# Kernel tuning notes

Hardware: AMD Instinct MI355X
Metric: run time of the kernel (lower is better)

The kernel has to match this reference:

```python
import jax, jax.numpy as jnp
import numpy as np

N_NODES = 100000
N_EDGES = 1600000
VOCAB = 15000
D_IN = 128
D_HID = 128
N_GRAPHS = 16


def setup_inputs() -> dict:
    key = jax.random.key(0)
    ks = jax.random.split(key, 16)
    stdv = 1.0 / np.sqrt(D_HID)
    inp = {
        "word_ids": jax.random.randint(ks[0], (N_NODES,), 0, VOCAB),
        "edge_src": jax.random.randint(ks[1], (N_EDGES,), 0, N_NODES),
        "edge_dst": jax.random.randint(ks[2], (N_EDGES,), 0, N_NODES),
        "edge_weight": jax.random.uniform(ks[3], (N_EDGES,), dtype=jnp.float32),
        "norm": jax.random.uniform(ks[4], (N_NODES,), dtype=jnp.float32),
        "graph_id": jnp.sort(jax.random.randint(ks[5], (N_NODES,), 0, N_GRAPHS)),
        "y_data": jax.random.uniform(ks[6], (N_GRAPHS,), dtype=jnp.float32),
        # learned params
        "word_embeds": jax.random.normal(ks[7], (VOCAB, D_IN), dtype=jnp.float32) * 0.05,
        "W0": jax.random.uniform(ks[8], (D_IN, D_HID), minval=-stdv, maxval=stdv, dtype=jnp.float32),
        "b0": jax.random.uniform(ks[9], (D_HID,), minval=-stdv, maxval=stdv, dtype=jnp.float32),
        "W1": jax.random.uniform(ks[10], (D_HID, D_HID), minval=-stdv, maxval=stdv, dtype=jnp.float32),
        "b1": jax.random.uniform(ks[11], (D_HID,), minval=-stdv, maxval=stdv, dtype=jnp.float32),
        "Wout": jax.random.uniform(ks[12], (D_HID, 1), minval=-stdv, maxval=stdv, dtype=jnp.float32),
        "bout": jax.random.uniform(ks[13], (1,), minval=-stdv, maxval=stdv, dtype=jnp.float32),
    }
    return inp


def _gcn_layer(h, W, b, norm, edge_src, edge_dst, edge_weight):
    # h: [N, d_in] -> [N, d_out]
    h = h @ W                                   # dense projection
    h = h * norm[:, None]                       # pre-aggregation norm
    msg = h[edge_src] * edge_weight[:, None]    # u_mul_e   [E, d]
    h = jax.ops.segment_sum(msg, edge_dst, num_segments=N_NODES)  # sum agg
    h = h * norm[:, None]                       # post-aggregation norm
    return jax.nn.relu(h + b)


def reference(word_ids, edge_src, edge_dst, edge_weight, norm, graph_id, y_data,
              word_embeds, W0, b0, W1, b1, Wout, bout):
    h = word_embeds[word_ids]                   # [N, D_IN]
    h = _gcn_layer(h, W0, b0, norm, edge_src, edge_dst, edge_weight)
    h = _gcn_layer(h, W1, b1, norm, edge_src, edge_dst, edge_weight)
    # per-graph max pooling (dgl.max_nodes)
    g = jax.ops.segment_max(h, graph_id, num_segments=N_GRAPHS)   # [B, D_HID]
    z = g @ Wout + bout                          # [B, 1] logits
    zf = z.reshape(-1)
    # binary_cross_entropy_with_logits, mean reduction (numerically stable)
    loss = jnp.mean(jnp.maximum(zf, 0.0) - zf * y_data + jnp.log1p(jnp.exp(-jnp.abs(zf))))
    y_pred = jax.nn.sigmoid(z)
    return loss, y_pred
```

## Files before the change

### kernel.cpp

```cpp
#include <hip/hip_runtime.h>
#include <math.h>

#define D 128
#define NG 16
#define NBINS 512
#define CHUNK 2048
#define CAPB 4608

typedef unsigned int uint;
typedef unsigned short ushort;
typedef unsigned long long u64;
typedef __attribute__((ext_vector_type(8))) short bf16x8;
typedef __attribute__((ext_vector_type(4))) float f32x4;

__device__ __forceinline__ ushort f32_to_bf16(float f) {
    uint b = __float_as_uint(f);
    b += 0x7fffu + ((b >> 16) & 1u);
    return (ushort)(b >> 16);
}
__device__ __forceinline__ uint pack_bf16x2(float lo, float hi) {
    return (uint)f32_to_bf16(lo) | ((uint)f32_to_bf16(hi) << 16);
}

__global__ __launch_bounds__(256) void k_binA(
    const int* __restrict__ esrc, const int* __restrict__ edst,
    const float* __restrict__ ew, const float* __restrict__ norm,
    u64* __restrict__ binned, int* __restrict__ loc_off,
    int* __restrict__ bin_cnt, int ne, int width)
{
    __shared__ int hist[NBINS], lscan[NBINS], lcur[NBINS];
    __shared__ int ws4[4];
    __shared__ u64 stage[CHUNK];
    const int tid = threadIdx.x;
    const int base = blockIdx.x * CHUNK;
    const int count = min(CHUNK, ne - base);

    hist[tid] = 0; hist[tid + 256] = 0;
    __syncthreads();

    int s[8], bn[8], dl[8]; float c[8];
    #pragma unroll
    for (int i = 0; i < 8; ++i) {
        int li = i * 256 + tid;
        bn[i] = -1;
        if (li < count) {
            int e = base + li;
            s[i] = esrc[e];
            int d = edst[e];
            bn[i] = d / width;
            dl[i] = d - bn[i] * width;
            c[i] = ew[e] * norm[s[i]];
            atomicAdd(&hist[bn[i]], 1);
        }
    }
    __syncthreads();

    {
        int lane = tid & 63, w = tid >> 6;
        int h0 = hist[2 * tid], h1 = hist[2 * tid + 1];
        int sum = h0 + h1, x = sum;
        for (int dlt = 1; dlt < 64; dlt <<= 1) {
            int t2 = __shfl_up(x, dlt);
            if (lane >= dlt) x += t2;
        }
        if (lane == 63) ws4[w] = x;
        __syncthreads();
        if (tid == 0) { int run = 0; for (int i = 0; i < 4; ++i) { int t3 = ws4[i]; ws4[i] = run; run += t3; } }
        __syncthreads();
        int b0 = ws4[w] + (x - sum);
        lscan[2 * tid] = b0;       lscan[2 * tid + 1] = b0 + h0;
        lcur[2 * tid] = b0;        lcur[2 * tid + 1] = b0 + h0;
    }
    __syncthreads();

    int* lo = loc_off + (size_t)blockIdx.x * (NBINS + 1);
    lo[tid] = lscan[tid]; lo[tid + 256] = lscan[tid + 256];
    if (tid == 0) lo[NBINS] = count;
    if (hist[tid])       atomicAdd(&bin_cnt[tid], hist[tid]);
    if (hist[tid + 256]) atomicAdd(&bin_cnt[tid + 256], hist[tid + 256]);

    #pragma unroll
    for (int i = 0; i < 8; ++i) {
        if (bn[i] >= 0) {
            int pos = atomicAdd(&lcur[bn[i]], 1);
            uint packed = (uint)s[i] | ((uint)dl[i] << 24);
            stage[pos] = ((u64)__float_as_uint(c[i]) << 32) | packed;
        }
    }
    __syncthreads();

    u64* outp = binned + (size_t)blockIdx.x * CHUNK;
    for (int j = tid; j < count; j += 256) outp[j] = stage[j];
}

__global__ __launch_bounds__(1024) void k_scan_top(int* __restrict__ bsum, int nb)
{
    int tid = threadIdx.x, lane = tid & 63, w = tid >> 6;
    int v = tid < nb ? bsum[tid] : 0;
    int x = v;
    for (int d = 1; d < 64; d <<= 1) {
        int t = __shfl_up(x, d);
        if (lane >= d) x += t;
    }
    __shared__ int ws[16];
    if (lane == 63) ws[w] = x;
    __syncthreads();
    if (tid == 0) { int run = 0; for (int i = 0; i < 16; ++i) { int t = ws[i]; ws[i] = run; run += t; } }
    __syncthreads();
    x += ws[w];
    if (tid < nb) bsum[tid] = x - v;
}

__global__ __launch_bounds__(256) void k_binB(
    const u64* __restrict__ binned, const int* __restrict__ loc_off,
    const int* __restrict__ bin_off, int* __restrict__ off,
    int2* __restrict__ csr, int n, int ne, int width, int nA)
{
    __shared__ u64 stA[CAPB];
    __shared__ int hist[256], cur[256];
    __shared__ int wsum[4];
    __shared__ int sTotal;
    const int tid = threadIdx.x;
    const int bin = blockIdx.x;
    const int d0 = bin * width;
    const int dcount = min(n - d0, width);
    const int base = bin_off[bin];

    if (tid == 0) sTotal = 0;
    hist[tid] = 0;
    __syncthreads();

    if (dcount > 0) {
        for (int f = tid; f < nA; f += 256) {
            const int* lo = loc_off + (size_t)f * (NBINS + 1);
            int a = lo[bin], b = lo[bin + 1];
            int len = b - a;
            if (len > 0) {
                int st = atomicAdd(&sTotal, len);
                const u64* src = binned + (size_t)f * CHUNK + a;
                for (int k = 0; k < len; ++k) {
                    u64 r = src[k];
                    stA[st + k] = r;
                    atomicAdd(&hist[(int)((r >> 24) & 0xFF)], 1);
                }
            }
        }
    }
    __syncthreads();
    const int cnt = sTotal;

    {
        int lane = tid & 63, w = tid >> 6;
        int v = hist[tid], x = v;
        for (int dlt = 1; dlt < 64; dlt <<= 1) {
            int t2 = __shfl_up(x, dlt);
            if (lane >= dlt) x += t2;
        }
        if (lane == 63) wsum[w] = x;
        __syncthreads();
        if (tid == 0) { int run = 0; for (int i = 0; i < 4; ++i) { int t3 = wsum[i]; wsum[i] = run; run += t3; } }
        __syncthreads();
        int ex = wsum[w] + x - v;
        cur[tid] = ex;
        if (tid < dcount) off[d0 + tid] = base + ex;
    }
    if (tid == 0 && dcount > 0 && d0 + dcount == n) off[n] = base + cnt;
    __syncthreads();

    for (int i = tid; i < cnt; i += 256) {
        u64 r = stA[i];
        int dl = (int)((r >> 24) & 0xFF);
        int pos = atomicAdd(&cur[dl], 1);
        csr[base + pos] = make_int2((int)(r & 0xFFFFFF), (int)(r >> 32));
    }
}

__global__ __launch_bounds__(256) void k_cvt_bf16(
    const float* __restrict__ src, ushort* __restrict__ dst, int nelem)
{
    int i = (blockIdx.x * 256 + threadIdx.x) * 4;
    if (i + 3 < nelem) {
        float4 v = *reinterpret_cast<const float4*>(src + i);
        ushort4 o;
        o.x = f32_to_bf16(v.x); o.y = f32_to_bf16(v.y);
        o.z = f32_to_bf16(v.z); o.w = f32_to_bf16(v.w);
        *reinterpret_cast<ushort4*>(dst + i) = o;
    } else {
        for (int k = 0; k < 4 && i + k < nelem; ++k) dst[i + k] = f32_to_bf16(src[i + k]);
    }
}

__global__ __launch_bounds__(256) void k_wfrag(
    const float* __restrict__ W, ushort* __restrict__ Wf)
{
    int t = blockIdx.x * 256 + threadIdx.x;
    if (t >= 2048) return;
    int lane = t & 63, tile = t >> 6;
    int ks = tile & 3, nt = tile >> 2;
    int col = nt * 16 + (lane & 15);
    int k0 = ks * 32 + (lane >> 4) * 8;
    ushort* dst = Wf + (size_t)t * 8;
    #pragma unroll
    for (int j = 0; j < 8; ++j)
        dst[j] = f32_to_bf16(W[(k0 + j) * D + col]);
}

__global__ __launch_bounds__(256) void k_agg_bf16(
    const int* __restrict__ off, const int2* __restrict__ csr,
    const int* __restrict__ wid, const ushort* __restrict__ tab,
    ushort* __restrict__ outbf, int n)
{
    int row = blockIdx.x * 8 + (threadIdx.x >> 5);
    if (row >= n) return;
    int q = threadIdx.x & 31;
    int h = q >> 4;
    int c8 = (q & 15) * 8;
    int j0 = off[row], j1 = off[row + 1];
    float acc[8] = {0.f, 0.f, 0.f, 0.f, 0.f, 0.f, 0.f, 0.f};

    for (int jb = j0; jb < j1; jb += 32) {
        int m = min(32, j1 - jb);
        int2 p = make_int2(0, 0);
        if (q < m) {
            p = csr[jb + q];
            if (wid) p.x = wid[p.x];
        }
        int t = 0;
        for (; t + 8 <= m; t += 8) {
            uint4 u[4]; float wv[4];
            #pragma unroll
            for (int k = 0; k < 4; ++k) {
                int eh = t + 2 * k + h;
                int sv = __shfl(p.x, eh, 32);
                wv[k] = __int_as_float(__shfl(p.y, eh, 32));
                u[k] = *reinterpret_cast<const uint4*>(tab + (size_t)sv * D + c8);
            }
            #pragma unroll
            for (int k = 0; k < 4; ++k) {
                acc[0] = fmaf(__uint_as_float(u[k].x << 16),          wv[k], acc[0]);
                acc[1] = fmaf(__uint_as_float(u[k].x & 0xffff0000u),  wv[k], acc[1]);
                acc[2] = fmaf(__uint_as_float(u[k].y << 16),          wv[k], acc[2]);
                acc[3] = fmaf(__uint_as_float(u[k].y & 0xffff0000u),  wv[k], acc[3]);
                acc[4] = fmaf(__uint_as_float(u[k].z << 16),          wv[k], acc[4]);
                acc[5] = fmaf(__uint_as_float(u[k].z & 0xffff0000u),  wv[k], acc[5]);
                acc[6] = fmaf(__uint_as_float(u[k].w << 16),          wv[k], acc[6]);
                acc[7] = fmaf(__uint_as_float(u[k].w & 0xffff0000u),  wv[k], acc[7]);
            }
        }
        for (; t < m; t += 2) {
            int eh = t + h;
            int sv = __shfl(p.x, eh, 32);
            float wvv = __int_as_float(__shfl(p.y, eh, 32));
            uint4 u = *reinterpret_cast<const uint4*>(tab + (size_t)sv * D + c8);
            acc[0] = fmaf(__uint_as_float(u.x << 16),         wvv, acc[0]);
            acc[1] = fmaf(__uint_as_float(u.x & 0xffff0000u), wvv, acc[1]);
            acc[2] = fmaf(__uint_as_float(u.y << 16),         wvv, acc[2]);
            acc[3] = fmaf(__uint_as_float(u.y & 0xffff0000u), wvv, acc[3]);
            acc[4] = fmaf(__uint_as_float(u.z << 16),         wvv, acc[4]);
            acc[5] = fmaf(__uint_as_float(u.z & 0xffff0000u), wvv, acc[5]);
            acc[6] = fmaf(__uint_as_float(u.w << 16),         wvv, acc[6]);
            acc[7] = fmaf(__uint_as_float(u.w & 0xffff0000u), wvv, acc[7]);
        }
    }
    #pragma unroll
    for (int i = 0; i < 8; ++i) acc[i] += __shfl_xor(acc[i], 16, 32);
    if (h == 0) {
        uint4 o;
        o.x = pack_bf16x2(acc[0], acc[1]);
        o.y = pack_bf16x2(acc[2], acc[3]);
        o.z = pack_bf16x2(acc[4], acc[5]);
        o.w = pack_bf16x2(acc[6], acc[7]);
        *reinterpret_cast<uint4*>(outbf + (size_t)row * D + c8) = o;
    }
}

__device__ __forceinline__ void gemm_core_16x128(
    const ushort* __restrict__ aggbf, const ushort* __restrict__ Wf,
    int rowbase, int lane, int n, f32x4 acc[8])
{
    int arow = rowbase + (lane & 15);
    const bf16x8* WfV = reinterpret_cast<const bf16x8*>(Wf);
    #pragma unroll
    for (int ks = 0; ks < 4; ++ks) {
        bf16x8 af = {0, 0, 0, 0, 0, 0, 0, 0};
        if (arow < n) {
            int k0 = ks * 32 + (lane >> 4) * 8;
            af = *reinterpret_cast<const bf16x8*>(aggbf + (size_t)arow * D + k0);
        }
        #pragma unroll
        for (int nt = 0; nt < 8; ++nt) {
            bf16x8 bf = WfV[(nt * 4 + ks) * 64 + lane];
            acc[nt] = __builtin_amdgcn_mfma_f32_16x16x32_bf16(af, bf, acc[nt], 0, 0, 0);
        }
    }
}

__global__ __launch_bounds__(256) void k_gemm_mfma_post(
    const ushort* __restrict__ aggbf, const ushort* __restrict__ Wf,
    const float* __restrict__ norm, const float* __restrict__ b,
    ushort* __restrict__ outbf, int n)
{
    int lane = threadIdx.x & 63;
    int w = threadIdx.x >> 6;
    int rowbase = blockIdx.x * 64 + w * 16;
    f32x4 acc[8] = {};
    gemm_core_16x128(aggbf, Wf, rowbase, lane, n, acc);

    int r0 = rowbase + (lane >> 4) * 4;
    float nrm[4];
    #pragma unroll
    for (int i = 0; i < 4; ++i) nrm[i] = (r0 + i < n) ? norm[r0 + i] : 0.f;
    #pragma unroll
    for (int nt = 0; nt < 8; ++nt) {
        int col = nt * 16 + (lane & 15);
        float bc = b[col];
        #pragma unroll
        for (int i = 0; i < 4; ++i) {
            int r = r0 + i;
            if (r < n) {
                float v = fmaxf(fmaf(acc[nt][i], nrm[i], bc), 0.f);
                outbf[(size_t)r * D + col] = f32_to_bf16(v);
            }
        }
    }
}

__global__ __launch_bounds__(256) void k_gemm_mfma_segmax(
    const ushort* __restrict__ aggbf, const ushort* __restrict__ Wf,
    const float* __restrict__ norm, const float* __restrict__ b,
    const int* __restrict__ gid, unsigned* __restrict__ g, int n)
{
    __shared__ float sh[64][132];
    __shared__ int sgid[64];
    int lane = threadIdx.x & 63;
    int w = threadIdx.x >> 6;
    int rowbase = blockIdx.x * 64 + w * 16;
    f32x4 acc[8] = {};
    gemm_core_16x128(aggbf, Wf, rowbase, lane, n, acc);

    int r0 = rowbase + (lane >> 4) * 4;
    int lr0 = w * 16 + (lane >> 4) * 4;
    float nrm[4];
    #pragma unroll
    for (int i = 0; i < 4; ++i) nrm[i] = (r0 + i < n) ? norm[r0 + i] : 0.f;
    #pragma unroll
    for (int nt = 0; nt < 8; ++nt) {
        int col = nt * 16 + (lane & 15);
        float bc = b[col];
        #pragma unroll
        for (int i = 0; i < 4; ++i) {
            float v = (r0 + i < n) ? fmaxf(fmaf(acc[nt][i], nrm[i], bc), 0.f) : 0.f;
            sh[lr0 + i][col] = v;
        }
    }
    if (threadIdx.x < 64) {
        int r = blockIdx.x * 64 + threadIdx.x;
        sgid[threadIdx.x] = (r < n) ? gid[r] : -1;
    }
    __syncthreads();

    if (threadIdx.x < D) {
        int c = threadIdx.x;
        int glo = 0x7fffffff, ghi = -1;
        #pragma unroll
        for (int i = 0; i < 64; ++i) {
            int gv = sgid[i];
            if (gv >= 0) { glo = min(glo, gv); ghi = max(ghi, gv); }
        }
        for (int gr = glo; gr <= ghi; ++gr) {
            float m = 0.f;
            #pragma unroll
            for (int i = 0; i < 64; ++i)
                if (sgid[i] == gr) m = fmaxf(m, sh[i][c]);
            if (m > 0.f) atomicMax(&g[gr * D + c], __float_as_uint(m));
        }
    }
}

__global__ __launch_bounds__(1024) void k_final(
    const unsigned* __restrict__ g, const float* __restrict__ Wout,
    const float* __restrict__ bout, const float* __restrict__ y,
    float* __restrict__ out)
{
    __shared__ float zs[NG];
    int wave = threadIdx.x >> 6, lane = threadIdx.x & 63;
    float acc = 0.f;
    for (int c = lane; c < D; c += 64)
        acc += __uint_as_float(g[wave * D + c]) * Wout[c];
    for (int off2 = 32; off2; off2 >>= 1) acc += __shfl_down(acc, off2);
    if (lane == 0) {
        float z = acc + bout[0];
        zs[wave] = z;
        out[1 + wave] = 1.f / (1.f + expf(-z));
    }
    __syncthreads();
    if (threadIdx.x == 0) {
        float loss = 0.f;
        for (int i = 0; i < NG; ++i) {
            float z = zs[i];
            loss += fmaxf(z, 0.f) - z * y[i] + log1pf(expf(-fabsf(z)));
        }
        out[0] = loss / NG;
    }
}

extern "C" void kernel_launch(void* const* d_in, const int* in_sizes, int n_in,
                              void* d_out, int out_size, void* d_ws, size_t ws_size,
                              hipStream_t stream) {
    const int*   word_ids = (const int*)  d_in[0];
    const int*   esrc     = (const int*)  d_in[1];
    const int*   edst     = (const int*)  d_in[2];
    const float* ew       = (const float*)d_in[3];
    const float* norm     = (const float*)d_in[4];
    const int*   gid      = (const int*)  d_in[5];
    const float* y        = (const float*)d_in[6];
    const float* embeds   = (const float*)d_in[7];
    const float* W0       = (const float*)d_in[8];
    const float* b0       = (const float*)d_in[9];
    const float* W1       = (const float*)d_in[10];
    const float* b1       = (const float*)d_in[11];
    const float* Wout     = (const float*)d_in[12];
    const float* bout     = (const float*)d_in[13];

    const int n  = in_sizes[0];
    const int ne = in_sizes[1];
    const int vocab = in_sizes[7] / D;
    float* out = (float*)d_out;

    const int nA = (ne + CHUNK - 1) / CHUNK;
    const int width = (n + NBINS - 1) / NBINS;

    ushort* aggbf = (ushort*)d_ws;
    int*    off   = (int*)(aggbf + (size_t)n * D);
    int*    bcnt  = off + (n + 1);
    int*    loff  = bcnt + NBINS;
    uintptr_t bin_addr = ((uintptr_t)(loff + (size_t)nA * (NBINS + 1)) + 15) & ~(uintptr_t)15;
    u64*    binned = (u64*)bin_addr;
    int2*   csr   = (int2*)(binned + (size_t)nA * CHUNK);
    ushort* h1    = (ushort*)(csr + ne);
    ushort* emb16 = h1 + (size_t)n * D;
    unsigned* g   = (unsigned*)(emb16 + (size_t)vocab * D);
    uintptr_t wf_addr = ((uintptr_t)(g + NG * D) + 15) & ~(uintptr_t)15;
    ushort* w0f = (ushort*)wf_addr;
    ushort* w1f = w0f + D * D;

    const dim3 blk(256);
    const int ablocks = (n + 7) / 8;
    const int mblocks = (n + 63) / 64;

    hipMemsetAsync(bcnt, 0, NBINS * sizeof(int), stream);
    k_binA<<<nA, blk, 0, stream>>>(esrc, edst, ew, norm, binned, loff, bcnt, ne, width);
    k_scan_top<<<1, 1024, 0, stream>>>(bcnt, NBINS);
    k_binB<<<NBINS, blk, 0, stream>>>(binned, loff, bcnt, off, csr, n, ne, width, nA);

    k_cvt_bf16<<<(vocab * D / 4 + 255) / 256, blk, 0, stream>>>(embeds, emb16, vocab * D);
    k_wfrag<<<8, blk, 0, stream>>>(W0, w0f);
    k_wfrag<<<8, blk, 0, stream>>>(W1, w1f);

    k_agg_bf16<<<ablocks, blk, 0, stream>>>(off, csr, word_ids, emb16, aggbf, n);
    k_gemm_mfma_post<<<mblocks, blk, 0, stream>>>(aggbf, w0f, norm, b0, h1, n);

    k_agg_bf16<<<ablocks, blk, 0, stream>>>(off, csr, nullptr, h1, aggbf, n);
    hipMemsetAsync(g, 0, NG * D * sizeof(unsigned), stream);
    k_gemm_mfma_segmax<<<mblocks, blk, 0, stream>>>(aggbf, w1f, norm, b1, gid, g, n);

    k_final<<<1, 1024, 0, stream>>>(g, Wout, bout, y, out);
}
```

Baseline: 259.8 us.

## Quantize layer-1 activations to int8 with per-row scales for second aggregation

The first GEMM epilogue now computes a per-row max, writes int8-quantized activations plus a float scale per row instead of bf16. A new aggregation kernel gathers the int8 rows, dequantizes with the source row's scale folded into the edge weight, and accumulates in fp32. This halves the bytes gathered per edge in the second message-passing pass, which is dominated by random row reads. The cost is reduced precision (int8, ReLU outputs only) and an extra scale load per edge.

```diff
diff --git a/kernel.cpp b/kernel.cpp
--- a/kernel.cpp
+++ b/kernel.cpp
@@ -20,6 +20,9 @@
 }
 __device__ __forceinline__ uint pack_bf16x2(float lo, float hi) {
     return (uint)f32_to_bf16(lo) | ((uint)f32_to_bf16(hi) << 16);
+}
+__device__ __forceinline__ float sb(uint u) {
+    return (float)(int)(signed char)(u & 0xffu);
 }
 
 __global__ __launch_bounds__(256) void k_binA(
@@ -274,6 +277,74 @@
     }
 }
 
+__global__ __launch_bounds__(256) void k_agg_q8(
+    const int* __restrict__ off, const int2* __restrict__ csr,
+    const char* __restrict__ tab8, const float* __restrict__ scale,
+    ushort* __restrict__ outbf, int n)
+{
+    int row = blockIdx.x * 8 + (threadIdx.x >> 5);
+    if (row >= n) return;
+    int q = threadIdx.x & 31;
+    int h = q >> 4;
+    int c8 = (q & 15) * 8;
+    int j0 = off[row], j1 = off[row + 1];
+    float acc[8] = {0.f, 0.f, 0.f, 0.f, 0.f, 0.f, 0.f, 0.f};
+
+    for (int jb = j0; jb < j1; jb += 32) {
+        int m = min(32, j1 - jb);
+        int2 p = make_int2(0, 0);
+        if (q < m) p = csr[jb + q];
+        int t = 0;
+        for (; t + 8 <= m; t += 8) {
+            uint2 u[4]; float wv[4];
+            #pragma unroll
+            for (int k = 0; k < 4; ++k) {
+                int eh = t + 2 * k + h;
+                int sv = __shfl(p.x, eh, 32);
+                float wc = __int_as_float(__shfl(p.y, eh, 32));
+                wv[k] = wc * scale[sv];
+                u[k] = *reinterpret_cast<const uint2*>(tab8 + (size_t)sv * D + c8);
+            }
+            #pragma unroll
+            for (int k = 0; k < 4; ++k) {
+                acc[0] = fmaf(sb(u[k].x),       wv[k], acc[0]);
+                acc[1] = fmaf(sb(u[k].x >> 8),  wv[k], acc[1]);
+                acc[2] = fmaf(sb(u[k].x >> 16), wv[k], acc[2]);
+                acc[3] = fmaf(sb(u[k].x >> 24), wv[k], acc[3]);
+                acc[4] = fmaf(sb(u[k].y),       wv[k], acc[4]);
+                acc[5] = fmaf(sb(u[k].y >> 8),  wv[k], acc[5]);
+                acc[6] = fmaf(sb(u[k].y >> 16), wv[k], acc[6]);
+                acc[7] = fmaf(sb(u[k].y >> 24), wv[k], acc[7]);
+            }
+        }
+        for (; t < m; t += 2) {
+            int eh = t + h;
+            int sv = __shfl(p.x, eh, 32);
+            float wc = __int_as_float(__shfl(p.y, eh, 32));
+            float wvv = wc * scale[sv];
+            uint2 u = *reinterpret_cast<const uint2*>(tab8 + (size_t)sv * D + c8);
+            acc[0] = fmaf(sb(u.x),       wvv, acc[0]);
+            acc[1] = fmaf(sb(u.x >> 8),  wvv, acc[1]);
+            acc[2] = fmaf(sb(u.x >> 16), wvv, acc[2]);
+            acc[3] = fmaf(sb(u.x >> 24), wvv, acc[3]);
+            acc[4] = fmaf(sb(u.y),       wvv, acc[4]);
+            acc[5] = fmaf(sb(u.y >> 8),  wvv, acc[5]);
+            acc[6] = fmaf(sb(u.y >> 16), wvv, acc[6]);
+            acc[7] = fmaf(sb(u.y >> 24), wvv, acc[7]);
+        }
+    }
+    #pragma unroll
+    for (int i = 0; i < 8; ++i) acc[i] += __shfl_xor(acc[i], 16, 32);
+    if (h == 0) {
+        uint4 o;
+        o.x = pack_bf16x2(acc[0], acc[1]);
+        o.y = pack_bf16x2(acc[2], acc[3]);
+        o.z = pack_bf16x2(acc[4], acc[5]);
+        o.w = pack_bf16x2(acc[6], acc[7]);
+        *reinterpret_cast<uint4*>(outbf + (size_t)row * D + c8) = o;
+    }
+}
+
 __device__ __forceinline__ void gemm_core_16x128(
     const ushort* __restrict__ aggbf, const ushort* __restrict__ Wf,
     int rowbase, int lane, int n, f32x4 acc[8])
@@ -295,10 +366,10 @@
     }
 }
 
-__global__ __launch_bounds__(256) void k_gemm_mfma_post(
+__global__ __launch_bounds__(256) void k_gemm_mfma_post_q8(
     const ushort* __restrict__ aggbf, const ushort* __restrict__ Wf,
     const float* __restrict__ norm, const float* __restrict__ b,
-    ushort* __restrict__ outbf, int n)
+    char* __restrict__ out8, float* __restrict__ scale, int n)
 {
     int lane = threadIdx.x & 63;
     int w = threadIdx.x >> 6;
@@ -310,16 +381,41 @@
     float nrm[4];
     #pragma unroll
     for (int i = 0; i < 4; ++i) nrm[i] = (r0 + i < n) ? norm[r0 + i] : 0.f;
+
+    float v[8][4];
+    float mx[4] = {0.f, 0.f, 0.f, 0.f};
+    #pragma unroll
+    for (int nt = 0; nt < 8; ++nt) {
+        float bc = b[nt * 16 + (lane & 15)];
+        #pragma unroll
+        for (int i = 0; i < 4; ++i) {
+            float t = fmaxf(fmaf(acc[nt][i], nrm[i], bc), 0.f);
+            v[nt][i] = t;
+            mx[i] = fmaxf(mx[i], t);
+        }
+    }
+    #pragma unroll
+    for (int d = 1; d < 16; d <<= 1) {
+        #pragma unroll
+        for (int i = 0; i < 4; ++i) mx[i] = fmaxf(mx[i], __shfl_xor(mx[i], d, 64));
+    }
+    float inv[4];
+    #pragma unroll
+    for (int i = 0; i < 4; ++i) inv[i] = (mx[i] > 0.f) ? 127.f / mx[i] : 0.f;
+    if ((lane & 15) == 0) {
+        #pragma unroll
+        for (int i = 0; i < 4; ++i)
+            if (r0 + i < n) scale[r0 + i] = (mx[i] > 0.f) ? mx[i] * (1.f / 127.f) : 0.f;
+    }
     #pragma unroll
     for (int nt = 0; nt < 8; ++nt) {
         int col = nt * 16 + (lane & 15);
-        float bc = b[col];
         #pragma unroll
         for (int i = 0; i < 4; ++i) {
             int r = r0 + i;
             if (r < n) {
-                float v = fmaxf(fmaf(acc[nt][i], nrm[i], bc), 0.f);
-                outbf[(size_t)r * D + col] = f32_to_bf16(v);
+                int qv = __float2int_rn(v[nt][i] * inv[i]);
+                out8[(size_t)r * D + col] = (char)min(qv, 127);
             }
         }
     }
@@ -437,8 +533,9 @@
     uintptr_t bin_addr = ((uintptr_t)(loff + (size_t)nA * (NBINS + 1)) + 15) & ~(uintptr_t)15;
     u64*    binned = (u64*)bin_addr;
     int2*   csr   = (int2*)(binned + (size_t)nA * CHUNK);
-    ushort* h1    = (ushort*)(csr + ne);
-    ushort* emb16 = h1 + (size_t)n * D;
+    char*   h1q   = (char*)(csr + ne);
+    float*  hscale = (float*)(h1q + (size_t)n * D);
+    ushort* emb16 = (ushort*)(hscale + n);
     unsigned* g   = (unsigned*)(emb16 + (size_t)vocab * D);
     uintptr_t wf_addr = ((uintptr_t)(g + NG * D) + 15) & ~(uintptr_t)15;
     ushort* w0f = (ushort*)wf_addr;
@@ -458,9 +555,9 @@
     k_wfrag<<<8, blk, 0, stream>>>(W1, w1f);
 
     k_agg_bf16<<<ablocks, blk, 0, stream>>>(off, csr, word_ids, emb16, aggbf, n);
-    k_gemm_mfma_post<<<mblocks, blk, 0, stream>>>(aggbf, w0f, norm, b0, h1, n);
-
-    k_agg_bf16<<<ablocks, blk, 0, stream>>>(off, csr, nullptr, h1, aggbf, n);
+    k_gemm_mfma_post_q8<<<mblocks, blk, 0, stream>>>(aggbf, w0f, norm, b0, h1q, hscale, n);
+
+    k_agg_q8<<<ablocks, blk, 0, stream>>>(off, csr, h1q, hscale, aggbf, n);
     hipMemsetAsync(g, 0, NG * D * sizeof(unsigned), stream);
     k_gemm_mfma_segmax<<<mblocks, blk, 0, stream>>>(aggbf, w1f, norm, b1, gid, g, n);
 
```

Result: faster. 226.8 us (-12.7%).
